# Performance work log

Measured on AMD Instinct MI355X. Metric: run time of the kernel, lower is better.

## Reference

```python
import jax, jax.numpy as jnp
import numpy as np

B, T, C, H = 8, 1024, 768, 12
D = C // H


def setup_inputs() -> dict:
    key = jax.random.key(0)
    ks = jax.random.split(key, 12)
    s = lambda fan_in: 1.0 / np.sqrt(fan_in)
    return {
        "x": jax.random.normal(ks[0], (B, T, C), dtype=jnp.float32),
        "ln_w": jnp.ones((C,), jnp.float32),
        "ln_b": jnp.zeros((C,), jnp.float32),
        "w_qkv": jax.random.normal(ks[1], (C, 3 * C), jnp.float32) * s(C),
        "b_qkv": jax.random.normal(ks[2], (3 * C,), jnp.float32) * 0.02,
        "w_out": jax.random.normal(ks[3], (C, C), jnp.float32) * s(C),
        "b_out": jax.random.normal(ks[4], (C,), jnp.float32) * 0.02,
        "w_c1": jax.random.normal(ks[5], (C, 4 * C), jnp.float32) * s(C),
        "b_c1": jax.random.normal(ks[6], (4 * C,), jnp.float32) * 0.02,
        "w_c2": jax.random.normal(ks[7], (4 * C, C), jnp.float32) * s(4 * C),
        "b_c2": jax.random.normal(ks[8], (C,), jnp.float32) * 0.02,
    }


def _layer_norm(x, w, b, eps=1e-5):
    mu = jnp.mean(x, axis=-1, keepdims=True)
    var = jnp.var(x, axis=-1, keepdims=True)
    return (x - mu) * jax.lax.rsqrt(var + eps) * w + b


def reference(x, ln_w, ln_b, w_qkv, b_qkv, w_out, b_out, w_c1, b_c1, w_c2, b_c2):
    b, t, c = x.shape
    # NOTE: both norms in Block share the SAME params (source re-assigns self.layer_norm)
    h = _layer_norm(x, ln_w, ln_b)
    qkv = h @ w_qkv + b_qkv  # [b,t,3c]
    # source splits as (k, q, v) in that order
    k, q, v = jnp.split(qkv, 3, axis=-1)
    k = k.reshape(b, t, H, D).transpose(0, 2, 1, 3)  # [b,h,t,d]
    q = q.reshape(b, t, H, D).transpose(0, 2, 1, 3)
    v = v.reshape(b, t, H, D).transpose(0, 2, 1, 3)
    # NOTE: no 1/sqrt(d) scaling in the source
    scores = jnp.einsum("bhqd,bhkd->bhqk", q, k)
    mask = jnp.tril(jnp.ones((t, t), dtype=bool))
    scores = jnp.where(mask, scores, -jnp.inf)
    attn = jax.nn.softmax(scores, axis=-1)
    y = jnp.einsum("bhqk,bhkd->bhqd", attn, v)
    y = y.transpose(0, 2, 1, 3).reshape(b, t, c)
    y = y @ w_out + b_out
    x = x + y
    h = _layer_norm(x, ln_w, ln_b)
    m = jax.nn.gelu(h @ w_c1 + b_c1, approximate=False) @ w_c2 + b_c2
    return x + m
```

## Files before the change

kernel.cpp:

```cpp
#include <hip/hip_runtime.h>
#include <hip/hip_bf16.h>
#include <math.h>

typedef short v4s __attribute__((ext_vector_type(4)));
typedef short v8s __attribute__((ext_vector_type(8)));
typedef float v4f __attribute__((ext_vector_type(4)));
typedef unsigned short us8 __attribute__((ext_vector_type(8)));

#if __has_builtin(__builtin_amdgcn_mfma_f32_16x16x16bf16_1k)
#define MFMA16(a, b, c) __builtin_amdgcn_mfma_f32_16x16x16bf16_1k(a, b, c, 0, 0, 0)
#else
__device__ inline v4f mfma16_fb(v4s a, v4s b, v4f c) {
    v8s a8 = {a[0], a[1], a[2], a[3], 0, 0, 0, 0};
    v8s b8 = {b[0], b[1], b[2], b[3], 0, 0, 0, 0};
    return __builtin_amdgcn_mfma_f32_16x16x32_bf16(a8, b8, c, 0, 0, 0);
}
#define MFMA16(a, b, c) mfma16_fb(a, b, c)
#endif

#define MFMA32(a, b, c) __builtin_amdgcn_mfma_f32_16x16x32_bf16(a, b, c, 0, 0, 0)

__device__ inline unsigned short f2bf(float f) {
    __hip_bfloat16 h = __float2bfloat16(f);
    union { __hip_bfloat16 h; unsigned short u; } cv;
    cv.h = h;
    return cv.u;
}

__device__ inline void gld16(const void* g, void* l) {
    __builtin_amdgcn_global_load_lds((const __attribute__((address_space(1))) void*)g,
                                     (__attribute__((address_space(3))) void*)l, 16, 0, 0);
}

__device__ inline float gelu_fast(float v) {
    const float z2 = 1.5957691216057308f * (v + 0.044715f * v * v * v);
    return v / (1.0f + __expf(-z2));
}

__global__ __launch_bounds__(256) void transpose_cvt(const float* __restrict__ in,
                                                     unsigned short* __restrict__ out,
                                                     int R, int Cn) {
    __shared__ float t[32][33];
    const int tid = threadIdx.x;
    const int tx = tid & 31, ty = tid >> 5;
    const int bx = blockIdx.x, by = blockIdx.y;
#pragma unroll
    for (int i = 0; i < 4; ++i) {
        int r = by * 32 + ty + i * 8;
        int c = bx * 32 + tx;
        t[ty + i * 8][tx] = in[(size_t)r * Cn + c];
    }
    __syncthreads();
#pragma unroll
    for (int i = 0; i < 4; ++i) {
        out[(size_t)(bx * 32 + ty + i * 8) * R + by * 32 + tx] = f2bf(t[tx][ty + i * 8]);
    }
}

__global__ __launch_bounds__(256) void ln_row(const float* __restrict__ x,
                                              const float* __restrict__ lw,
                                              const float* __restrict__ lb,
                                              unsigned short* __restrict__ out) {
    const int row = blockIdx.x;
    const int tid = threadIdx.x;
    const float* xr = x + (size_t)row * 768;
    float v0 = xr[tid], v1 = xr[tid + 256], v2 = xr[tid + 512];
    float s = v0 + v1 + v2;
    float q = v0 * v0 + v1 * v1 + v2 * v2;
#pragma unroll
    for (int o = 1; o < 64; o <<= 1) {
        s += __shfl_xor(s, o);
        q += __shfl_xor(q, o);
    }
    __shared__ float rs[4], rq[4];
    const int w = tid >> 6;
    if ((tid & 63) == 0) { rs[w] = s; rq[w] = q; }
    __syncthreads();
    s = rs[0] + rs[1] + rs[2] + rs[3];
    q = rq[0] + rq[1] + rq[2] + rq[3];
    const float mean = s * (1.0f / 768.0f);
    const float var = q * (1.0f / 768.0f) - mean * mean;
    const float rstd = rsqrtf(var + 1e-5f);
    unsigned short* orow = out + (size_t)row * 768;
    orow[tid] = f2bf((v0 - mean) * rstd * lw[tid] + lb[tid]);
    orow[tid + 256] = f2bf((v1 - mean) * rstd * lw[tid + 256] + lb[tid + 256]);
    orow[tid + 512] = f2bf((v2 - mean) * rstd * lw[tid + 512] + lb[tid + 512]);
}

template <int EPI>
__global__ __launch_bounds__(256) void gemm_bf16(const unsigned short* __restrict__ A,
                                                 const unsigned short* __restrict__ BT,
                                                 const float* __restrict__ bias,
                                                 const float* __restrict__ resid,
                                                 void* __restrict__ outp,
                                                 int M, int N, int K) {
    __shared__ __align__(16) unsigned short As[128 * 64];
    __shared__ __align__(16) unsigned short Bs[128 * 64];
    const int tid = threadIdx.x;
    const int lane = tid & 63;
    const int w = tid >> 6;
    const int g = lane >> 4;
    const int c16 = lane & 15;
    const int row0 = blockIdx.x * 128;
    const int col0 = blockIdx.y * 128;
    const int wm = w & 1, wn = w >> 1;

    v4f acc[4][4];
#pragma unroll
    for (int m = 0; m < 4; ++m)
#pragma unroll
        for (int n = 0; n < 4; ++n) acc[m][n] = (v4f){0.f, 0.f, 0.f, 0.f};

    const unsigned short* ap[4];
    const unsigned short* bp[4];
#pragma unroll
    for (int i = 0; i < 4; ++i) {
        const int c = (i * 4 + w) * 64 + lane;
        const int r = c >> 3;
        const int dc = (c & 7) ^ (r & 7);
        ap[i] = A + (size_t)(row0 + r) * K + dc * 8;
        bp[i] = BT + (size_t)(col0 + r) * K + dc * 8;
    }

    const int nk = K >> 6;
    for (int kt = 0; kt < nk; ++kt) {
        __syncthreads();
#pragma unroll
        for (int i = 0; i < 4; ++i) {
            const int c = (i * 4 + w) * 64 + lane;
            gld16(ap[i], As + (size_t)c * 8);
            gld16(bp[i], Bs + (size_t)c * 8);
            ap[i] += 64;
            bp[i] += 64;
        }
        __syncthreads();
#pragma unroll
        for (int ks = 0; ks < 2; ++ks) {
            const int koff = ks * 64 + 16 * g;
            v8s af[4], bf[4];
#pragma unroll
            for (int m = 0; m < 4; ++m) {
                const int r = wm * 64 + m * 16 + c16;
                af[m] = *(const v8s*)((const char*)As + r * 128 + (koff ^ ((r & 7) << 4)));
            }
#pragma unroll
            for (int n = 0; n < 4; ++n) {
                const int r = wn * 64 + n * 16 + c16;
                bf[n] = *(const v8s*)((const char*)Bs + r * 128 + (koff ^ ((r & 7) << 4)));
            }
#pragma unroll
            for (int m = 0; m < 4; ++m)
#pragma unroll
                for (int n = 0; n < 4; ++n) acc[m][n] = MFMA32(af[m], bf[n], acc[m][n]);
        }
    }
#pragma unroll
    for (int m = 0; m < 4; ++m)
#pragma unroll
        for (int n = 0; n < 4; ++n)
#pragma unroll
            for (int r = 0; r < 4; ++r) {
                const int row = row0 + wm * 64 + m * 16 + 4 * g + r;
                const int col = col0 + wn * 64 + n * 16 + c16;
                float v = acc[m][n][r] + bias[col];
                if (EPI == 1) v += resid[(size_t)row * N + col];
                if (EPI == 2) v = gelu_fast(v);
                if (EPI == 1)
                    ((float*)outp)[(size_t)row * N + col] = v;
                else
                    ((unsigned short*)outp)[(size_t)row * N + col] = f2bf(v);
            }
}

__global__ __launch_bounds__(256) void attn_kernel(const unsigned short* __restrict__ qkv,
                                                   unsigned short* __restrict__ y) {
    __shared__ __align__(16) unsigned short Ks[64 * 64];
    __shared__ __align__(16) unsigned short Vt[64 * 68];
    __shared__ __align__(16) unsigned short Ps[4][16 * 68];
    const int tid = threadIdx.x;
    const int lane = tid & 63;
    const int w = tid >> 6;
    const int g = lane >> 4;
    const int c16 = lane & 15;
    const int qt = gridDim.x - 1 - blockIdx.x;
    const int h = blockIdx.y, b = blockIdx.z;
    const int tok0 = b * 1024 + qt * 64;

    v4s qf[4];
    const unsigned short* qbase = qkv + (size_t)(tok0 + w * 16 + c16) * 2304 + 768 + h * 64;
#pragma unroll
    for (int ks = 0; ks < 4; ++ks) qf[ks] = *(const v4s*)(qbase + ks * 16 + 4 * g);

    v4f yacc[4];
#pragma unroll
    for (int d = 0; d < 4; ++d) yacc[d] = (v4f){0.f, 0.f, 0.f, 0.f};
    float mrun = -__builtin_inff();
    float lrun = 0.0f;
    const int qpos = qt * 64 + w * 16 + c16;

    for (int kt = 0; kt <= qt; ++kt) {
        const int tokk = b * 1024 + kt * 64;
        __syncthreads();
#pragma unroll
        for (int i = 0; i < 2; ++i) {
            const int c = (i * 4 + w) * 64 + lane;
            const int kk = c >> 3;
            const int dc = (c & 7) ^ (kk & 7);
            gld16(qkv + (size_t)(tokk + kk) * 2304 + h * 64 + dc * 8, Ks + (size_t)c * 8);
        }
#pragma unroll
        for (int it = 0; it < 2; ++it) {
            const int off = (it * 256 + tid) * 8;
            const int kk = off >> 6, d0 = off & 63;
            us8 vv = *(const us8*)(qkv + (size_t)(tokk + kk) * 2304 + 1536 + h * 64 + d0);
#pragma unroll
            for (int j = 0; j < 8; ++j) Vt[(d0 + j) * 68 + kk] = vv[j];
        }
        __syncthreads();

        v4f st[4];
#pragma unroll
        for (int kb = 0; kb < 4; ++kb) st[kb] = (v4f){0.f, 0.f, 0.f, 0.f};
#pragma unroll
        for (int ks = 0; ks < 4; ++ks) {
            const int koff = ks * 32 + 8 * g;
            v4s kf[4];
#pragma unroll
            for (int kb = 0; kb < 4; ++kb) {
                const int r = kb * 16 + c16;
                kf[kb] = *(const v4s*)((const char*)Ks + r * 128 + (koff ^ ((r & 7) << 4)));
            }
#pragma unroll
            for (int kb = 0; kb < 4; ++kb) st[kb] = MFMA16(kf[kb], qf[ks], st[kb]);
        }

        float pmax = -__builtin_inff();
        if (kt == qt) {
#pragma unroll
            for (int kb = 0; kb < 4; ++kb)
#pragma unroll
                for (int r = 0; r < 4; ++r) {
                    const int kkpos = kt * 64 + kb * 16 + 4 * g + r;
                    if (kkpos > qpos) st[kb][r] = -__builtin_inff();
                    pmax = fmaxf(pmax, st[kb][r]);
                }
        } else {
#pragma unroll
            for (int kb = 0; kb < 4; ++kb)
#pragma unroll
                for (int r = 0; r < 4; ++r) pmax = fmaxf(pmax, st[kb][r]);
        }
        pmax = fmaxf(pmax, __shfl_xor(pmax, 16));
        pmax = fmaxf(pmax, __shfl_xor(pmax, 32));
        const float mnew = fmaxf(mrun, pmax);
        const float scale = __expf(mrun - mnew);
        float psum = 0.0f;
#pragma unroll
        for (int kb = 0; kb < 4; ++kb) {
            v4s pw;
#pragma unroll
            for (int r = 0; r < 4; ++r) {
                const float pv = __expf(st[kb][r] - mnew);
                psum += pv;
                pw[r] = (short)f2bf(pv);
            }
            *(v4s*)((char*)&Ps[w][0] + c16 * 136 + kb * 32 + 8 * g) = pw;
        }
        psum += __shfl_xor(psum, 16);
        psum += __shfl_xor(psum, 32);
        lrun = lrun * scale + psum;
        mrun = mnew;

        float scr[4];
#pragma unroll
        for (int r = 0; r < 4; ++r) scr[r] = __shfl(scale, g * 4 + r);
#pragma unroll
        for (int d = 0; d < 4; ++d)
#pragma unroll
            for (int r = 0; r < 4; ++r) yacc[d][r] *= scr[r];

#pragma unroll
        for (int ks = 0; ks < 4; ++ks) {
            const v4s pf = *(const v4s*)((const char*)&Ps[w][0] + c16 * 136 + ks * 32 + 8 * g);
#pragma unroll
            for (int d = 0; d < 4; ++d) {
                const v4s vf =
                    *(const v4s*)((const char*)Vt + (d * 16 + c16) * 136 + ks * 32 + 8 * g);
                yacc[d] = MFMA16(pf, vf, yacc[d]);
            }
        }
    }

    const float inv = 1.0f / lrun;
    float invr[4];
#pragma unroll
    for (int r = 0; r < 4; ++r) invr[r] = __shfl(inv, g * 4 + r);
#pragma unroll
    for (int d = 0; d < 4; ++d)
#pragma unroll
        for (int r = 0; r < 4; ++r) {
            const int row = tok0 + w * 16 + 4 * g + r;
            const int col = h * 64 + d * 16 + c16;
            y[(size_t)row * 768 + col] = f2bf(yacc[d][r] * invr[r]);
        }
}

extern "C" void kernel_launch(void* const* d_in, const int* in_sizes, int n_in,
                              void* d_out, int out_size, void* d_ws, size_t ws_size,
                              hipStream_t stream) {
    const float* x = (const float*)d_in[0];
    const float* ln_w = (const float*)d_in[1];
    const float* ln_b = (const float*)d_in[2];
    const float* w_qkv = (const float*)d_in[3];
    const float* b_qkv = (const float*)d_in[4];
    const float* w_out = (const float*)d_in[5];
    const float* b_out = (const float*)d_in[6];
    const float* w_c1 = (const float*)d_in[7];
    const float* b_c1 = (const float*)d_in[8];
    const float* w_c2 = (const float*)d_in[9];
    const float* b_c2 = (const float*)d_in[10];
    float* out = (float*)d_out;

    char* ws = (char*)d_ws;
    unsigned short* wTqkv = (unsigned short*)(ws + 0);
    unsigned short* wTout = (unsigned short*)(ws + 3538944);
    unsigned short* wTc1 = (unsigned short*)(ws + 4718592);
    unsigned short* wTc2 = (unsigned short*)(ws + 9437184);
    unsigned short* hbuf = (unsigned short*)(ws + 14155776);
    unsigned short* qkvb = (unsigned short*)(ws + 26738688);
    unsigned short* ybuf = (unsigned short*)(ws + 64487424);
    float* x2 = (float*)(ws + 77070336);
    unsigned short* m1 = qkvb;

    transpose_cvt<<<dim3(2304 / 32, 768 / 32), 256, 0, stream>>>(w_qkv, wTqkv, 768, 2304);
    transpose_cvt<<<dim3(768 / 32, 768 / 32), 256, 0, stream>>>(w_out, wTout, 768, 768);
    transpose_cvt<<<dim3(3072 / 32, 768 / 32), 256, 0, stream>>>(w_c1, wTc1, 768, 3072);
    transpose_cvt<<<dim3(768 / 32, 3072 / 32), 256, 0, stream>>>(w_c2, wTc2, 3072, 768);

    ln_row<<<8192, 256, 0, stream>>>(x, ln_w, ln_b, hbuf);
    gemm_bf16<0><<<dim3(64, 18), 256, 0, stream>>>(hbuf, wTqkv, b_qkv, nullptr, qkvb, 8192, 2304, 768);
    attn_kernel<<<dim3(16, 12, 8), 256, 0, stream>>>(qkvb, ybuf);
    gemm_bf16<1><<<dim3(64, 6), 256, 0, stream>>>(ybuf, wTout, b_out, x, x2, 8192, 768, 768);
    ln_row<<<8192, 256, 0, stream>>>(x2, ln_w, ln_b, hbuf);
    gemm_bf16<2><<<dim3(64, 24), 256, 0, stream>>>(hbuf, wTc1, b_c1, nullptr, m1, 8192, 3072, 768);
    gemm_bf16<1><<<dim3(64, 6), 256, 0, stream>>>(m1, wTc2, b_c2, x2, out, 8192, 768, 3072);
}
```

Before: 405.3 us.

## Pair causal query tiles per attention block and use 16x16x32 MFMA for QK

Each attention block now handles two query tiles, p and 15-p, so every block does the same amount of causal work and each loaded K/V tile is shared by both queries. The grid halves to 8 blocks along x. QK^T now uses the 16x16x32 bf16 MFMA with 8-wide fragments, which halves the number of MFMA issues. In exchange, each block keeps two sets of accumulators, which raises register pressure, and there are fewer blocks to hide latency.

```diff
diff --git a/kernel.cpp b/kernel.cpp
--- a/kernel.cpp
+++ b/kernel.cpp
@@ -172,6 +172,79 @@
             }
 }
 
+__device__ inline void attn_tile(const unsigned short* Ks, const unsigned short* Vt,
+                                 unsigned short* Psw, const v8s* qf8, v4f* yacc,
+                                 float& mrun, float& lrun, bool diag, int mask0,
+                                 int g, int c16) {
+    v4f st[4];
+#pragma unroll
+    for (int kb = 0; kb < 4; ++kb) st[kb] = (v4f){0.f, 0.f, 0.f, 0.f};
+#pragma unroll
+    for (int ks = 0; ks < 2; ++ks) {
+        const int koff = ks * 64 + 16 * g;
+#pragma unroll
+        for (int kb = 0; kb < 4; ++kb) {
+            const int r = kb * 16 + c16;
+            const v8s kf = *(const v8s*)((const char*)Ks + r * 128 + (koff ^ ((r & 7) << 4)));
+            st[kb] = MFMA32(kf, qf8[ks], st[kb]);
+        }
+    }
+
+    float pmax = -__builtin_inff();
+    if (diag) {
+#pragma unroll
+        for (int kb = 0; kb < 4; ++kb)
+#pragma unroll
+            for (int r = 0; r < 4; ++r) {
+                if (kb * 16 + 4 * g + r > mask0) st[kb][r] = -__builtin_inff();
+                pmax = fmaxf(pmax, st[kb][r]);
+            }
+    } else {
+#pragma unroll
+        for (int kb = 0; kb < 4; ++kb)
+#pragma unroll
+            for (int r = 0; r < 4; ++r) pmax = fmaxf(pmax, st[kb][r]);
+    }
+    pmax = fmaxf(pmax, __shfl_xor(pmax, 16));
+    pmax = fmaxf(pmax, __shfl_xor(pmax, 32));
+    const float mnew = fmaxf(mrun, pmax);
+    const float scale = __expf(mrun - mnew);
+    float psum = 0.0f;
+#pragma unroll
+    for (int kb = 0; kb < 4; ++kb) {
+        v4s pw;
+#pragma unroll
+        for (int r = 0; r < 4; ++r) {
+            const float pv = __expf(st[kb][r] - mnew);
+            psum += pv;
+            pw[r] = (short)f2bf(pv);
+        }
+        *(v4s*)((char*)Psw + c16 * 136 + kb * 32 + 8 * g) = pw;
+    }
+    psum += __shfl_xor(psum, 16);
+    psum += __shfl_xor(psum, 32);
+    lrun = lrun * scale + psum;
+    mrun = mnew;
+
+    float scr[4];
+#pragma unroll
+    for (int r = 0; r < 4; ++r) scr[r] = __shfl(scale, g * 4 + r);
+#pragma unroll
+    for (int d = 0; d < 4; ++d)
+#pragma unroll
+        for (int r = 0; r < 4; ++r) yacc[d][r] *= scr[r];
+
+#pragma unroll
+    for (int ks = 0; ks < 4; ++ks) {
+        const v4s pf = *(const v4s*)((const char*)Psw + c16 * 136 + ks * 32 + 8 * g);
+#pragma unroll
+        for (int d = 0; d < 4; ++d) {
+            const v4s vf = *(const v4s*)((const char*)Vt + (d * 16 + c16) * 136 + ks * 32 + 8 * g);
+            yacc[d] = MFMA16(pf, vf, yacc[d]);
+        }
+    }
+}
+
 __global__ __launch_bounds__(256) void attn_kernel(const unsigned short* __restrict__ qkv,
                                                    unsigned short* __restrict__ y) {
     __shared__ __align__(16) unsigned short Ks[64 * 64];
@@ -182,23 +255,34 @@
     const int w = tid >> 6;
     const int g = lane >> 4;
     const int c16 = lane & 15;
-    const int qt = gridDim.x - 1 - blockIdx.x;
+    const int p = blockIdx.x;
     const int h = blockIdx.y, b = blockIdx.z;
-    const int tok0 = b * 1024 + qt * 64;
-
-    v4s qf[4];
-    const unsigned short* qbase = qkv + (size_t)(tok0 + w * 16 + c16) * 2304 + 768 + h * 64;
-#pragma unroll
-    for (int ks = 0; ks < 4; ++ks) qf[ks] = *(const v4s*)(qbase + ks * 16 + 4 * g);
-
-    v4f yacc[4];
-#pragma unroll
-    for (int d = 0; d < 4; ++d) yacc[d] = (v4f){0.f, 0.f, 0.f, 0.f};
-    float mrun = -__builtin_inff();
-    float lrun = 0.0f;
-    const int qpos = qt * 64 + w * 16 + c16;
-
-    for (int kt = 0; kt <= qt; ++kt) {
+    const int qtA = 15 - p, qtB = p;
+    const int tokA = b * 1024 + qtA * 64;
+    const int tokB = b * 1024 + qtB * 64;
+
+    v8s qfA[2], qfB[2];
+    {
+        const unsigned short* qbA = qkv + (size_t)(tokA + w * 16 + c16) * 2304 + 768 + h * 64;
+        const unsigned short* qbB = qkv + (size_t)(tokB + w * 16 + c16) * 2304 + 768 + h * 64;
+#pragma unroll
+        for (int ks = 0; ks < 2; ++ks) {
+            qfA[ks] = *(const v8s*)(qbA + ks * 32 + 8 * g);
+            qfB[ks] = *(const v8s*)(qbB + ks * 32 + 8 * g);
+        }
+    }
+
+    v4f yA[4], yB[4];
+#pragma unroll
+    for (int d = 0; d < 4; ++d) {
+        yA[d] = (v4f){0.f, 0.f, 0.f, 0.f};
+        yB[d] = (v4f){0.f, 0.f, 0.f, 0.f};
+    }
+    float mA = -__builtin_inff(), lA = 0.0f;
+    float mB = -__builtin_inff(), lB = 0.0f;
+    const int qrow = w * 16 + c16;
+
+    for (int kt = 0; kt <= qtA; ++kt) {
         const int tokk = b * 1024 + kt * 64;
         __syncthreads();
 #pragma unroll
@@ -218,91 +302,39 @@
         }
         __syncthreads();
 
-        v4f st[4];
-#pragma unroll
-        for (int kb = 0; kb < 4; ++kb) st[kb] = (v4f){0.f, 0.f, 0.f, 0.f};
-#pragma unroll
-        for (int ks = 0; ks < 4; ++ks) {
-            const int koff = ks * 32 + 8 * g;
-            v4s kf[4];
-#pragma unroll
-            for (int kb = 0; kb < 4; ++kb) {
-                const int r = kb * 16 + c16;
-                kf[kb] = *(const v4s*)((const char*)Ks + r * 128 + (koff ^ ((r & 7) << 4)));
-            }
-#pragma unroll
-            for (int kb = 0; kb < 4; ++kb) st[kb] = MFMA16(kf[kb], qf[ks], st[kb]);
-        }
-
-        float pmax = -__builtin_inff();
-        if (kt == qt) {
-#pragma unroll
-            for (int kb = 0; kb < 4; ++kb)
-#pragma unroll
-                for (int r = 0; r < 4; ++r) {
-                    const int kkpos = kt * 64 + kb * 16 + 4 * g + r;
-                    if (kkpos > qpos) st[kb][r] = -__builtin_inff();
-                    pmax = fmaxf(pmax, st[kb][r]);
-                }
-        } else {
-#pragma unroll
-            for (int kb = 0; kb < 4; ++kb)
-#pragma unroll
-                for (int r = 0; r < 4; ++r) pmax = fmaxf(pmax, st[kb][r]);
-        }
-        pmax = fmaxf(pmax, __shfl_xor(pmax, 16));
-        pmax = fmaxf(pmax, __shfl_xor(pmax, 32));
-        const float mnew = fmaxf(mrun, pmax);
-        const float scale = __expf(mrun - mnew);
-        float psum = 0.0f;
-#pragma unroll
-        for (int kb = 0; kb < 4; ++kb) {
-            v4s pw;
+        attn_tile(Ks, Vt, &Ps[w][0], qfA, yA, mA, lA, kt == qtA, qrow, g, c16);
+        if (kt <= qtB)
+            attn_tile(Ks, Vt, &Ps[w][0], qfB, yB, mB, lB, kt == qtB, qrow, g, c16);
+    }
+
+    {
+        const float inv = 1.0f / lA;
+        float invr[4];
+#pragma unroll
+        for (int r = 0; r < 4; ++r) invr[r] = __shfl(inv, g * 4 + r);
+#pragma unroll
+        for (int d = 0; d < 4; ++d)
 #pragma unroll
             for (int r = 0; r < 4; ++r) {
-                const float pv = __expf(st[kb][r] - mnew);
-                psum += pv;
-                pw[r] = (short)f2bf(pv);
-            }
-            *(v4s*)((char*)&Ps[w][0] + c16 * 136 + kb * 32 + 8 * g) = pw;
-        }
-        psum += __shfl_xor(psum, 16);
-        psum += __shfl_xor(psum, 32);
-        lrun = lrun * scale + psum;
-        mrun = mnew;
-
-        float scr[4];
-#pragma unroll
-        for (int r = 0; r < 4; ++r) scr[r] = __shfl(scale, g * 4 + r);
+                const int row = tokA + w * 16 + 4 * g + r;
+                const int col = h * 64 + d * 16 + c16;
+                y[(size_t)row * 768 + col] = f2bf(yA[d][r] * invr[r]);
+            }
+    }
+    {
+        const float inv = 1.0f / lB;
+        float invr[4];
+#pragma unroll
+        for (int r = 0; r < 4; ++r) invr[r] = __shfl(inv, g * 4 + r);
 #pragma unroll
         for (int d = 0; d < 4; ++d)
 #pragma unroll
-            for (int r = 0; r < 4; ++r) yacc[d][r] *= scr[r];
-
-#pragma unroll
-        for (int ks = 0; ks < 4; ++ks) {
-            const v4s pf = *(const v4s*)((const char*)&Ps[w][0] + c16 * 136 + ks * 32 + 8 * g);
-#pragma unroll
-            for (int d = 0; d < 4; ++d) {
-                const v4s vf =
-                    *(const v4s*)((const char*)Vt + (d * 16 + c16) * 136 + ks * 32 + 8 * g);
-                yacc[d] = MFMA16(pf, vf, yacc[d]);
-            }
-        }
-    }
-
-    const float inv = 1.0f / lrun;
-    float invr[4];
-#pragma unroll
-    for (int r = 0; r < 4; ++r) invr[r] = __shfl(inv, g * 4 + r);
-#pragma unroll
-    for (int d = 0; d < 4; ++d)
-#pragma unroll
-        for (int r = 0; r < 4; ++r) {
-            const int row = tok0 + w * 16 + 4 * g + r;
-            const int col = h * 64 + d * 16 + c16;
-            y[(size_t)row * 768 + col] = f2bf(yacc[d][r] * invr[r]);
-        }
+            for (int r = 0; r < 4; ++r) {
+                const int row = tokB + w * 16 + 4 * g + r;
+                const int col = h * 64 + d * 16 + c16;
+                y[(size_t)row * 768 + col] = f2bf(yB[d][r] * invr[r]);
+            }
+    }
 }
 
 extern "C" void kernel_launch(void* const* d_in, const int* in_sizes, int n_in,
@@ -339,7 +371,7 @@
 
     ln_row<<<8192, 256, 0, stream>>>(x, ln_w, ln_b, hbuf);
     gemm_bf16<0><<<dim3(64, 18), 256, 0, stream>>>(hbuf, wTqkv, b_qkv, nullptr, qkvb, 8192, 2304, 768);
-    attn_kernel<<<dim3(16, 12, 8), 256, 0, stream>>>(qkvb, ybuf);
+    attn_kernel<<<dim3(8, 12, 8), 256, 0, stream>>>(qkvb, ybuf);
     gemm_bf16<1><<<dim3(64, 6), 256, 0, stream>>>(ybuf, wTout, b_out, x, x2, 8192, 768, 768);
     ln_row<<<8192, 256, 0, stream>>>(x2, ln_w, ln_b, hbuf);
     gemm_bf16<2><<<dim3(64, 24), 256, 0, stream>>>(hbuf, wTc1, b_c1, nullptr, m1, 8192, 3072, 768);
```

After: 367.1 us. 1.1x faster.
